# Kernel optimization log

Hardware: AMD Instinct MI355X
Metric: run time of the kernel (lower is better)

The kernel has to match this reference:

```python
import jax, jax.numpy as jnp
import numpy as np

B, T, D = 16, 2048, 384
BLOCK = 3
NB = D // BLOCK
EPS = 1e-8


def setup_inputs() -> dict:
    key = jax.random.key(0)
    ks = jax.random.split(key, 8)
    std = 0.02
    quat_sequence = jax.random.normal(ks[0], (B, T, 4), dtype=jnp.float32)
    # weights stored as (in, out); x @ W
    W_in = jax.random.normal(ks[1], (4, D), dtype=jnp.float32) * std
    W_biv = jax.random.normal(ks[2], (D, NB * 3), dtype=jnp.float32) * (1.0 / np.sqrt(D))
    b_biv = jnp.zeros((NB * 3,), dtype=jnp.float32)
    W_dec = jax.random.normal(ks[3], (D, D), dtype=jnp.float32) * (1.0 / np.sqrt(D))
    b_dec = jnp.full((D,), 1.4, dtype=jnp.float32)
    W_inj = jax.random.normal(ks[4], (D, D), dtype=jnp.float32) * (1.0 / np.sqrt(D))
    b_inj = jax.random.normal(ks[5], (D,), dtype=jnp.float32) * (1.0 / np.sqrt(D))
    W_out = jax.random.normal(ks[6], (D, 4), dtype=jnp.float32) * std
    return {
        'quat_sequence': quat_sequence,
        'W_in': W_in, 'W_biv': W_biv, 'b_biv': b_biv,
        'W_dec': W_dec, 'b_dec': b_dec, 'W_inj': W_inj, 'b_inj': b_inj,
        'W_out': W_out,
    }


def _quat_rotate_blocks(h_blocks, bivectors):
    # h_blocks, bivectors: (..., NB, 3)
    norm_b = jnp.clip(jnp.linalg.norm(bivectors, axis=-1, keepdims=True), EPS, None)
    half = norm_b / 2
    w = jnp.cos(half)[..., 0]
    s = (jnp.sin(half) / norm_b)[..., 0]
    qx = s * bivectors[..., 2]
    qy = -s * bivectors[..., 1]
    qz = s * bivectors[..., 0]
    vx, vy, vz = h_blocks[..., 0], h_blocks[..., 1], h_blocks[..., 2]
    tx = 2 * (qy * vz - qz * vy)
    ty = 2 * (qz * vx - qx * vz)
    tz = 2 * (qx * vy - qy * vx)
    rx = vx + w * tx + (qy * tz - qz * ty)
    ry = vy + w * ty + (qz * tx - qx * tz)
    rz = vz + w * tz + (qx * ty - qy * tx)
    return jnp.stack([rx, ry, rz], axis=-1)


def reference(quat_sequence, W_in, W_biv, b_biv, W_dec, b_dec, W_inj, b_inj, W_out):
    hidden_input = quat_sequence @ W_in                       # (B,T,D)
    bivectors_all = (hidden_input @ W_biv + b_biv).reshape(B, T, NB, 3)
    decay_all = jax.nn.sigmoid(hidden_input @ W_dec + b_dec)  # (B,T,D)
    injection_all = hidden_input @ W_inj + b_inj              # (B,T,D)

    def step(h, xs):
        biv, dec, inj = xs  # (B,NB,3), (B,D), (B,D)
        rot = _quat_rotate_blocks(h.reshape(B, NB, 3), biv).reshape(B, D)
        h_next = dec * rot + inj
        return h_next, h_next

    h0 = jnp.zeros((B, D), dtype=quat_sequence.dtype)
    xs = (jnp.swapaxes(bivectors_all, 0, 1),
          jnp.swapaxes(decay_all, 0, 1),
          jnp.swapaxes(injection_all, 0, 1))
    _, hidden_seq = jax.lax.scan(step, h0, xs)                # (T,B,D)
    hidden_output = jnp.swapaxes(hidden_seq, 0, 1)            # (B,T,D)

    predicted_raw = hidden_output @ W_out                     # (B,T,4)
    norm = jnp.clip(jnp.linalg.norm(predicted_raw, axis=-1, keepdims=True), EPS, None)
    return predicted_raw / norm
```

## Files before the change

### kernel.cpp

```cpp
#include <hip/hip_runtime.h>
#include <hip/hip_bf16.h>
#include <hip/hip_fp16.h>

#define BB 16
#define TT 2048
#define DD 384
#define GG 2048
#define CC 256
#define LL 8
#define HSTRIDE (DD + 8)
#define EPSF 1e-8f
#define RCPF(x) __builtin_amdgcn_rcpf(x)


__global__ __launch_bounds__(256) void precompute_wc(
        const float* __restrict__ W_in,
        const float* __restrict__ W_biv,
        const float* __restrict__ W_dec,
        const float* __restrict__ W_inj,
        const float* __restrict__ b_biv,
        const float* __restrict__ b_dec,
        const float* __restrict__ b_inj,
        float* __restrict__ Wc) {
    int m = blockIdx.x;
    int jl = threadIdx.x & 15;
    int dp = threadIdx.x >> 4;
    int j = blockIdx.y * 16 + jl;
    const float* __restrict__ W = (m == 0) ? W_biv : (m == 1) ? W_dec : W_inj;
    float a[4] = {0.f, 0.f, 0.f, 0.f};
    for (int d = dp; d < DD; d += 16) {
        float wv = W[d * DD + j];
#pragma unroll
        for (int k = 0; k < 4; ++k) a[k] = fmaf(W_in[k * DD + d], wv, a[k]);
    }
    __shared__ float red[16][17][4];
#pragma unroll
    for (int k = 0; k < 4; ++k) red[dp][jl][k] = a[k];
    __syncthreads();
    for (int s = 8; s >= 1; s >>= 1) {
        if (dp < s) {
#pragma unroll
            for (int k = 0; k < 4; ++k) red[dp][jl][k] += red[dp + s][jl][k];
        }
        __syncthreads();
    }
    int n = j / 3, comp = j - 3 * n;
    if (dp < 4) {
        Wc[((m * 4 + dp) * 128 + n) * 4 + comp] = red[0][jl][dp];
    } else if (dp == 4) {
#pragma unroll
        for (int k = 0; k < 4; ++k) Wc[((m * 4 + k) * 128 + n) * 4 + 3] = 0.f;
        Wc[(1536 + m * 128 + n) * 4 + 3] = 0.f;
    } else if (dp == 5) {
        const float* bsrc = (m == 0) ? b_biv : (m == 1) ? b_dec : b_inj;
        Wc[(1536 + m * 128 + n) * 4 + comp] = bsrc[j];
    }
}

struct Wts {
    float wb[4][3], wd[4][3], wi[4][3];
    float bb[3], bd[3], bj[3];
};

__device__ __forceinline__ void load_wts(const float4* __restrict__ Wc4, int n, Wts& W) {
#pragma unroll
    for (int k = 0; k < 4; ++k) {
        float4 v = Wc4[(0 * 4 + k) * 128 + n];
        W.wb[k][0] = v.x; W.wb[k][1] = v.y; W.wb[k][2] = v.z;
    }
#pragma unroll
    for (int k = 0; k < 4; ++k) {
        float4 v = Wc4[(1 * 4 + k) * 128 + n];
        W.wd[k][0] = v.x; W.wd[k][1] = v.y; W.wd[k][2] = v.z;
    }
#pragma unroll
    for (int k = 0; k < 4; ++k) {
        float4 v = Wc4[(2 * 4 + k) * 128 + n];
        W.wi[k][0] = v.x; W.wi[k][1] = v.y; W.wi[k][2] = v.z;
    }
    float4 b0 = Wc4[1536 + 0 * 128 + n];
    float4 b1 = Wc4[1536 + 1 * 128 + n];
    float4 b2 = Wc4[1536 + 2 * 128 + n];
    W.bb[0] = b0.x; W.bb[1] = b0.y; W.bb[2] = b0.z;
    W.bd[0] = b1.x; W.bd[1] = b1.y; W.bd[2] = b1.z;
    W.bj[0] = b2.x; W.bj[1] = b2.y; W.bj[2] = b2.z;
}

#define DOTW(M, c, bias) \
    fmaf(q.w, W.M[3][c], fmaf(q.z, W.M[2][c], fmaf(q.y, W.M[1][c], fmaf(q.x, W.M[0][c], bias))))

__device__ __forceinline__ void step_parts(const Wts& W, float4 q,
        float& dec0, float& dec1, float& dec2,
        float& w, float& qx, float& qy, float& qz,
        float& i0, float& i1, float& i2) {
    float bx = DOTW(wb, 0, W.bb[0]);
    float by = DOTW(wb, 1, W.bb[1]);
    float bz = DOTW(wb, 2, W.bb[2]);
    float d0 = DOTW(wd, 0, W.bd[0]);
    float d1 = DOTW(wd, 1, W.bd[1]);
    float d2 = DOTW(wd, 2, W.bd[2]);
    i0 = DOTW(wi, 0, W.bj[0]);
    i1 = DOTW(wi, 1, W.bj[1]);
    i2 = DOTW(wi, 2, W.bj[2]);
    dec0 = RCPF(1.f + __expf(-d0));
    dec1 = RCPF(1.f + __expf(-d1));
    dec2 = RCPF(1.f + __expf(-d2));
    float u = fmaf(bx, bx, fmaf(by, by, bz * bz));
    w = fmaf(u, fmaf(u, 2.6041667e-3f, -0.125f), 1.f);
    float s = fmaf(u, fmaf(u, 2.6041667e-4f, -2.0833333e-2f), 0.5f);
    qx = s * bz; qy = -s * by; qz = s * bx;
}

__device__ __forceinline__ void step_matrix(const Wts& W, float4 q,
                                            float M[9], float& i0, float& i1, float& i2) {
    float dec0, dec1, dec2, w, qx, qy, qz;
    step_parts(W, q, dec0, dec1, dec2, w, qx, qy, qz, i0, i1, i2);
    float xx = qx*qx, yy = qy*qy, zz = qz*qz;
    float xy = qx*qy, xz = qx*qz, yz = qy*qz;
    float wxs = w*qx, wys = w*qy, wzs = w*qz;
    M[0] = dec0 * (1.f - 2.f*(yy+zz));
    M[1] = dec0 * (2.f*(xy - wzs));
    M[2] = dec0 * (2.f*(xz + wys));
    M[3] = dec1 * (2.f*(xy + wzs));
    M[4] = dec1 * (1.f - 2.f*(xx+zz));
    M[5] = dec1 * (2.f*(yz - wxs));
    M[6] = dec2 * (2.f*(xz - wys));
    M[7] = dec2 * (2.f*(yz + wxs));
    M[8] = dec2 * (1.f - 2.f*(xx+yy));
}

__device__ __forceinline__ void step_init12(const Wts& W, float4 q, float A[12]) {
    float M[9], i0, i1, i2;
    step_matrix(W, q, M, i0, i1, i2);
#pragma unroll
    for (int e = 0; e < 9; ++e) A[e] = M[e];
    A[9] = i0; A[10] = i1; A[11] = i2;
}

__device__ __forceinline__ void step_compose12(const Wts& W, float4 q, float A[12]) {
    float M[9], i0, i1, i2;
    step_matrix(W, q, M, i0, i1, i2);
    float n0 = fmaf(M[0], A[0], fmaf(M[1], A[3], M[2] * A[6]));
    float n1 = fmaf(M[0], A[1], fmaf(M[1], A[4], M[2] * A[7]));
    float n2 = fmaf(M[0], A[2], fmaf(M[1], A[5], M[2] * A[8]));
    float n3 = fmaf(M[3], A[0], fmaf(M[4], A[3], M[5] * A[6]));
    float n4 = fmaf(M[3], A[1], fmaf(M[4], A[4], M[5] * A[7]));
    float n5 = fmaf(M[3], A[2], fmaf(M[4], A[5], M[5] * A[8]));
    float n6 = fmaf(M[6], A[0], fmaf(M[7], A[3], M[8] * A[6]));
    float n7 = fmaf(M[6], A[1], fmaf(M[7], A[4], M[8] * A[7]));
    float n8 = fmaf(M[6], A[2], fmaf(M[7], A[5], M[8] * A[8]));
    float n9  = fmaf(M[0], A[9], fmaf(M[1], A[10], fmaf(M[2], A[11], i0)));
    float n10 = fmaf(M[3], A[9], fmaf(M[4], A[10], fmaf(M[5], A[11], i1)));
    float n11 = fmaf(M[6], A[9], fmaf(M[7], A[10], fmaf(M[8], A[11], i2)));
    A[0]=n0; A[1]=n1; A[2]=n2; A[3]=n3; A[4]=n4; A[5]=n5;
    A[6]=n6; A[7]=n7; A[8]=n8; A[9]=n9; A[10]=n10; A[11]=n11;
}

__device__ __forceinline__ void step_apply(const Wts& W, float4 q,
                                           float& vx, float& vy, float& vz) {
    float dec0, dec1, dec2, w, qx, qy, qz, i0, i1, i2;
    step_parts(W, q, dec0, dec1, dec2, w, qx, qy, qz, i0, i1, i2);
    float tx = 2.f * (qy * vz - qz * vy);
    float ty = 2.f * (qz * vx - qx * vz);
    float tz = 2.f * (qx * vy - qy * vx);
    float rx = vx + w * tx + (qy * tz - qz * ty);
    float ry = vy + w * ty + (qz * tx - qx * tz);
    float rz = vz + w * tz + (qx * ty - qy * tx);
    vx = fmaf(dec0, rx, i0);
    vy = fmaf(dec1, ry, i1);
    vz = fmaf(dec2, rz, i2);
}

#define COMPOSE(R, C, P)                                                    \
    R[0] = fmaf(C[0], P[0], fmaf(C[1], P[3], C[2] * P[6]));                 \
    R[1] = fmaf(C[0], P[1], fmaf(C[1], P[4], C[2] * P[7]));                 \
    R[2] = fmaf(C[0], P[2], fmaf(C[1], P[5], C[2] * P[8]));                 \
    R[3] = fmaf(C[3], P[0], fmaf(C[4], P[3], C[5] * P[6]));                 \
    R[4] = fmaf(C[3], P[1], fmaf(C[4], P[4], C[5] * P[7]));                 \
    R[5] = fmaf(C[3], P[2], fmaf(C[4], P[5], C[5] * P[8]));                 \
    R[6] = fmaf(C[6], P[0], fmaf(C[7], P[3], C[8] * P[6]));                 \
    R[7] = fmaf(C[6], P[1], fmaf(C[7], P[4], C[8] * P[7]));                 \
    R[8] = fmaf(C[6], P[2], fmaf(C[7], P[5], C[8] * P[8]));                 \
    R[9]  = fmaf(C[0], P[9], fmaf(C[1], P[10], fmaf(C[2], P[11], C[9])));   \
    R[10] = fmaf(C[3], P[9], fmaf(C[4], P[10], fmaf(C[5], P[11], C[10])));  \
    R[11] = fmaf(C[6], P[9], fmaf(C[7], P[10], fmaf(C[8], P[11], C[11])));

__global__ __launch_bounds__(128) void chunk_compose(
        const float* __restrict__ quat,
        const float4* __restrict__ Wc4,
        float4* __restrict__ AffH) {
    int c = blockIdx.x, b = blockIdx.y, n = threadIdx.x;
    int g = b * 128 + n;

    const float4* __restrict__ qp = (const float4*)(quat + (size_t)b * TT * 4) + c * LL;
    float4 q[LL];
#pragma unroll
    for (int t = 0; t < LL; ++t) q[t] = qp[t];

    Wts W;
    load_wts(Wc4, n, W);

    float A[12];
    step_init12(W, q[0], A);
#pragma unroll
    for (int t = 1; t < LL; ++t) step_compose12(W, q[t], A);

    union { __half2 h2[8]; float4 f4[2]; } u;
#pragma unroll
    for (int e = 0; e < 6; ++e) u.h2[e] = __floats2half2_rn(A[2 * e], A[2 * e + 1]);
    u.h2[6] = __floats2half2_rn(0.f, 0.f);
    u.h2[7] = __floats2half2_rn(0.f, 0.f);
    float4* o = AffH + ((size_t)c * GG + g) * 2;
    o[0] = u.f4[0];
    o[1] = u.f4[1];
}

__global__ __launch_bounds__(256) void chunk_scan(
        const float4* __restrict__ AffH,
        float4* __restrict__ Hs) {
    int g = (blockIdx.x * 256 + threadIdx.x) >> 6;
    int l = threadIdx.x & 63;

    float m[4][12];
#pragma unroll
    for (int k = 0; k < 4; ++k) {
        const float4* a = AffH + ((size_t)(4 * l + k) * GG + g) * 2;
        union { __half2 h2[8]; float4 f4[2]; } u;
        u.f4[0] = a[0]; u.f4[1] = a[1];
#pragma unroll
        for (int e = 0; e < 6; ++e) {
            float2 v = __half22float2(u.h2[e]);
            m[k][2 * e] = v.x; m[k][2 * e + 1] = v.y;
        }
    }
    float q01[12], q012[12], Q[12];
    COMPOSE(q01, m[1], m[0]);
    COMPOSE(q012, m[2], q01);
    COMPOSE(Q, m[3], q012);

    float P[12];
#pragma unroll
    for (int k = 0; k < 12; ++k) P[k] = __shfl_up(Q[k], 1);
    if (l == 0) {
        P[0]=1.f; P[1]=0.f; P[2]=0.f; P[3]=0.f; P[4]=1.f; P[5]=0.f;
        P[6]=0.f; P[7]=0.f; P[8]=1.f; P[9]=0.f; P[10]=0.f; P[11]=0.f;
    }
#pragma unroll
    for (int sft = 1; sft < 64; sft <<= 1) {
        float S[12], N[12];
#pragma unroll
        for (int k = 0; k < 12; ++k) S[k] = __shfl_up(P[k], sft);
        COMPOSE(N, P, S);
        bool act = (l >= sft);
#pragma unroll
        for (int k = 0; k < 12; ++k) P[k] = act ? N[k] : P[k];
    }

    float h0 = P[9], h1 = P[10], h2 = P[11];
#pragma unroll
    for (int k = 0; k < 4; ++k) {
        Hs[(size_t)(4 * l + k) * GG + g] = make_float4(h0, h1, h2, 0.f);
        if (k < 3) {
            float n0 = fmaf(m[k][0], h0, fmaf(m[k][1], h1, fmaf(m[k][2], h2, m[k][9])));
            float n1 = fmaf(m[k][3], h0, fmaf(m[k][4], h1, fmaf(m[k][5], h2, m[k][10])));
            float n2 = fmaf(m[k][6], h0, fmaf(m[k][7], h1, fmaf(m[k][8], h2, m[k][11])));
            h0 = n0; h1 = n1; h2 = n2;
        }
    }
}

__global__ __launch_bounds__(128) void chunk_apply_out(
        const float* __restrict__ quat,
        const float4* __restrict__ Wc4,
        const float* __restrict__ W_out,
        const float4* __restrict__ Hs,
        float* __restrict__ out) {
    int c = blockIdx.x, b = blockIdx.y, n = threadIdx.x;
    int g = b * 128 + n;

    const float4* __restrict__ qp = (const float4*)(quat + (size_t)b * TT * 4) + c * LL;
    float4 q[LL];
#pragma unroll
    for (int t = 0; t < LL; ++t) q[t] = qp[t];

    float4 h4 = Hs[(size_t)c * GG + g];

    Wts W;
    load_wts(Wc4, n, W);

    __shared__ float H[LL][HSTRIDE];

    int j0 = 3 * n;
    float vx = h4.x, vy = h4.y, vz = h4.z;
#pragma unroll
    for (int t = 0; t < LL; ++t) {
        step_apply(W, q[t], vx, vy, vz);
        H[t][j0] = vx; H[t][j0 + 1] = vy; H[t][j0 + 2] = vz;
    }
    __syncthreads();

    int r = n >> 4, p = n & 15;
    float s0 = 0.f, s1 = 0.f, s2 = 0.f, s3 = 0.f;
#pragma unroll 8
    for (int j = 0; j < DD / 16; ++j) {
        int d = p + 16 * j;
        float hv = H[r][d];
        float4 wv = *(const float4*)(W_out + (size_t)d * 4);
        s0 = fmaf(hv, wv.x, s0);
        s1 = fmaf(hv, wv.y, s1);
        s2 = fmaf(hv, wv.z, s2);
        s3 = fmaf(hv, wv.w, s3);
    }
#pragma unroll
    for (int off = 1; off <= 8; off <<= 1) {
        s0 += __shfl_xor(s0, off);
        s1 += __shfl_xor(s1, off);
        s2 += __shfl_xor(s2, off);
        s3 += __shfl_xor(s3, off);
    }
    if (p == 0) {
        float norm = fmaxf(sqrtf(fmaf(s0, s0, fmaf(s1, s1, fmaf(s2, s2, s3 * s3)))), EPSF);
        float inv = RCPF(norm);
        float* outp = out + ((size_t)b * TT + (size_t)c * LL + r) * 4;
        *(float4*)outp = make_float4(s0 * inv, s1 * inv, s2 * inv, s3 * inv);
    }
}

extern "C" void kernel_launch(void* const* d_in, const int* in_sizes, int n_in,
                              void* d_out, int out_size, void* d_ws, size_t ws_size,
                              hipStream_t stream) {
    const float* quat  = (const float*)d_in[0];
    const float* W_in  = (const float*)d_in[1];
    const float* W_biv = (const float*)d_in[2];
    const float* b_biv = (const float*)d_in[3];
    const float* W_dec = (const float*)d_in[4];
    const float* b_dec = (const float*)d_in[5];
    const float* W_inj = (const float*)d_in[6];
    const float* b_inj = (const float*)d_in[7];
    const float* W_out = (const float*)d_in[8];
    float* out = (float*)d_out;

    const size_t AFF_OFF = 32768;
    const size_t AFF_B   = (size_t)CC * GG * 32;
    const size_t HS_OFF  = AFF_OFF + AFF_B;

    float*  Wc   = (float*)d_ws;
    float4* Wc4  = (float4*)d_ws;
    float4* AffH = (float4*)((char*)d_ws + AFF_OFF);
    float4* Hs   = (float4*)((char*)d_ws + HS_OFF);

    precompute_wc<<<dim3(3, DD / 16), dim3(256), 0, stream>>>(
        W_in, W_biv, W_dec, W_inj, b_biv, b_dec, b_inj, Wc);
    chunk_compose<<<dim3(CC, BB), dim3(128), 0, stream>>>(quat, Wc4, AffH);
    chunk_scan<<<dim3(GG / 4), dim3(256), 0, stream>>>(AffH, Hs);
    chunk_apply_out<<<dim3(CC, BB), dim3(128), 0, stream>>>(quat, Wc4, W_out, Hs, out);
}
```

Measured before the change: 59.83 us.

## Use shorter chunks with more chunks per lane in the scan

Halves the chunk length from 8 to 4 timesteps, which doubles the chunk count to 512. Each lane of the chunk scan now composes 8 chunk affines serially before the 64-lane shuffle scan. The affine buffer is transposed to group-major layout so each lane reads its 8 chunks contiguously. The apply kernel now has more blocks, each doing less sequential work, and its output reduction is re-split across 32 lanes per row. In exchange, the intermediate affine and hidden-state buffers double in size and the chunk scan does more serial composition per lane.

```diff
diff --git a/kernel.cpp b/kernel.cpp
--- a/kernel.cpp
+++ b/kernel.cpp
@@ -6,8 +6,9 @@
 #define TT 2048
 #define DD 384
 #define GG 2048
-#define CC 256
-#define LL 8
+#define CC 512
+#define LL 4
+#define OCT 8
 #define HSTRIDE (DD + 8)
 #define EPSF 1e-8f
 #define RCPF(x) __builtin_amdgcn_rcpf(x)
@@ -210,7 +211,7 @@
     for (int e = 0; e < 6; ++e) u.h2[e] = __floats2half2_rn(A[2 * e], A[2 * e + 1]);
     u.h2[6] = __floats2half2_rn(0.f, 0.f);
     u.h2[7] = __floats2half2_rn(0.f, 0.f);
-    float4* o = AffH + ((size_t)c * GG + g) * 2;
+    float4* o = AffH + ((size_t)g * CC + c) * 2;
     o[0] = u.f4[0];
     o[1] = u.f4[1];
 }
@@ -221,10 +222,10 @@
     int g = (blockIdx.x * 256 + threadIdx.x) >> 6;
     int l = threadIdx.x & 63;
 
-    float m[4][12];
-#pragma unroll
-    for (int k = 0; k < 4; ++k) {
-        const float4* a = AffH + ((size_t)(4 * l + k) * GG + g) * 2;
+    float m[OCT][12];
+#pragma unroll
+    for (int k = 0; k < OCT; ++k) {
+        const float4* a = AffH + ((size_t)g * CC + (OCT * l + k)) * 2;
         union { __half2 h2[8]; float4 f4[2]; } u;
         u.f4[0] = a[0]; u.f4[1] = a[1];
 #pragma unroll
@@ -233,10 +234,15 @@
             m[k][2 * e] = v.x; m[k][2 * e + 1] = v.y;
         }
     }
-    float q01[12], q012[12], Q[12];
-    COMPOSE(q01, m[1], m[0]);
-    COMPOSE(q012, m[2], q01);
-    COMPOSE(Q, m[3], q012);
+    float Q[12], Tq[12];
+#pragma unroll
+    for (int e = 0; e < 12; ++e) Q[e] = m[0][e];
+#pragma unroll
+    for (int k = 1; k < OCT; ++k) {
+        COMPOSE(Tq, m[k], Q);
+#pragma unroll
+        for (int e = 0; e < 12; ++e) Q[e] = Tq[e];
+    }
 
     float P[12];
 #pragma unroll
@@ -258,9 +264,9 @@
 
     float h0 = P[9], h1 = P[10], h2 = P[11];
 #pragma unroll
-    for (int k = 0; k < 4; ++k) {
-        Hs[(size_t)(4 * l + k) * GG + g] = make_float4(h0, h1, h2, 0.f);
-        if (k < 3) {
+    for (int k = 0; k < OCT; ++k) {
+        Hs[(size_t)(OCT * l + k) * GG + g] = make_float4(h0, h1, h2, 0.f);
+        if (k < OCT - 1) {
             float n0 = fmaf(m[k][0], h0, fmaf(m[k][1], h1, fmaf(m[k][2], h2, m[k][9])));
             float n1 = fmaf(m[k][3], h0, fmaf(m[k][4], h1, fmaf(m[k][5], h2, m[k][10])));
             float n2 = fmaf(m[k][6], h0, fmaf(m[k][7], h1, fmaf(m[k][8], h2, m[k][11])));
@@ -299,11 +305,11 @@
     }
     __syncthreads();
 
-    int r = n >> 4, p = n & 15;
+    int r = n >> 5, p = n & 31;
     float s0 = 0.f, s1 = 0.f, s2 = 0.f, s3 = 0.f;
-#pragma unroll 8
-    for (int j = 0; j < DD / 16; ++j) {
-        int d = p + 16 * j;
+#pragma unroll
+    for (int j = 0; j < DD / 32; ++j) {
+        int d = p + 32 * j;
         float hv = H[r][d];
         float4 wv = *(const float4*)(W_out + (size_t)d * 4);
         s0 = fmaf(hv, wv.x, s0);
@@ -312,7 +318,7 @@
         s3 = fmaf(hv, wv.w, s3);
     }
 #pragma unroll
-    for (int off = 1; off <= 8; off <<= 1) {
+    for (int off = 1; off <= 16; off <<= 1) {
         s0 += __shfl_xor(s0, off);
         s1 += __shfl_xor(s1, off);
         s2 += __shfl_xor(s2, off);
```

New measurement: 66.09 us. 10.5% more time.
